# Optimization experiments

Measured on AMD Instinct MI355X. Metric: run time of the kernel, lower is better.

Reference implementation:

```python
import jax, jax.numpy as jnp
import numpy as np

N = 50000      # nodes
E = 800000     # edges (before self loops)
IN = 128       # input feature dim
HID = 64       # hidden channels per head
H = 4          # heads
OUT = 1        # final out channels
D1 = H * HID   # 256, concat feature dim
NEG_SLOPE = 0.2


def _p(k, shape):
    return jax.random.normal(k, shape, jnp.float32) * 0.1


def setup_inputs() -> dict:
    key = jax.random.key(0)
    ks = jax.random.split(key, 32)
    inp = {
        "x": jax.random.normal(ks[0], (N, IN), jnp.float32),
        "edge_index": jax.random.randint(ks[1], (2, E), 0, N, dtype=jnp.int32),
        "batch": jnp.zeros((N,), jnp.int32),
    }
    # layer 0: GATConv(IN -> HID, heads=H, concat) ; Linear(IN -> H*HID)
    inp["cW0"] = _p(ks[2], (IN, H * HID)); inp["cas0"] = _p(ks[3], (H, HID))
    inp["cad0"] = _p(ks[4], (H, HID));     inp["cb0"] = jnp.zeros((D1,), jnp.float32)
    inp["lW0"] = _p(ks[5], (IN, D1));      inp["lb0"] = jnp.zeros((D1,), jnp.float32)
    # layer 1: GATConv(D1 -> HID, heads=H, concat) ; Linear(D1 -> D1)
    inp["cW1"] = _p(ks[6], (D1, H * HID)); inp["cas1"] = _p(ks[7], (H, HID))
    inp["cad1"] = _p(ks[8], (H, HID));     inp["cb1"] = jnp.zeros((D1,), jnp.float32)
    inp["lW1"] = _p(ks[9], (D1, D1));      inp["lb1"] = jnp.zeros((D1,), jnp.float32)
    # layer 2: GATConv(D1 -> OUT, heads=H, concat=False -> mean) ; Linear(D1 -> OUT)
    inp["cW2"] = _p(ks[10], (D1, H * OUT)); inp["cas2"] = _p(ks[11], (H, OUT))
    inp["cad2"] = _p(ks[12], (H, OUT));     inp["cb2"] = jnp.zeros((OUT,), jnp.float32)
    inp["lW2"] = _p(ks[13], (D1, OUT));     inp["lb2"] = jnp.zeros((OUT,), jnp.float32)
    return inp


def gat_conv(x, W, att_src, att_dst, bias, src, dst, out_c, concat):
    """PyG-style GATConv with self loops already included in (src, dst)."""
    n = x.shape[0]
    xl = (x @ W).reshape(n, H, out_c)                  # [N,H,C]
    a_s = (xl * att_src).sum(-1)                       # [N,H]
    a_d = (xl * att_dst).sum(-1)                       # [N,H]
    e = jax.nn.leaky_relu(a_s[src] + a_d[dst], NEG_SLOPE)   # [Et,H]
    # numerically stable segment softmax over destination nodes
    e_max = jax.ops.segment_max(e, dst, num_segments=n)
    ex = jnp.exp(e - e_max[dst])
    denom = jax.ops.segment_sum(ex, dst, num_segments=n)
    alpha = ex / (denom[dst] + 1e-16)                  # [Et,H]
    msg = xl[src] * alpha[..., None]                   # [Et,H,C]
    out = jax.ops.segment_sum(msg, dst, num_segments=n)  # [N,H,C]
    out = out.reshape(n, H * out_c) if concat else out.mean(axis=1)
    return out + bias


def _forward(x, edge_index,
             cW0, cas0, cad0, cb0, lW0, lb0,
             cW1, cas1, cad1, cb1, lW1, lb1,
             cW2, cas2, cad2, cb2, lW2, lb2):
    n = x.shape[0]
    loop = jnp.arange(n, dtype=edge_index.dtype)
    src = jnp.concatenate([edge_index[0], loop])
    dst = jnp.concatenate([edge_index[1], loop])
    h = jax.nn.elu(gat_conv(x, cW0, cas0, cad0, cb0, src, dst, HID, True) + (x @ lW0 + lb0))
    h = jax.nn.elu(gat_conv(h, cW1, cas1, cad1, cb1, src, dst, HID, True) + (h @ lW1 + lb1))
    return gat_conv(h, cW2, cas2, cad2, cb2, src, dst, OUT, False) + (h @ lW2 + lb2)


def reference(x, edge_index, batch,
              cW0, cas0, cad0, cb0, lW0, lb0,
              cW1, cas1, cad1, cb1, lW1, lb1,
              cW2, cas2, cad2, cb2, lW2, lb2):
    return _forward(x, edge_index,
                    cW0, cas0, cad0, cb0, lW0, lb0,
                    cW1, cas1, cad1, cb1, lW1, lb1,
                    cW2, cas2, cad2, cb2, lW2, lb2)
```

## Files before the change

### kernel.cpp

```cpp
#include <hip/hip_runtime.h>
#include <cstddef>
#include <cstdint>

#define NN 50000
#define EE 800000
#define ET_ (EE + NN)

typedef __attribute__((ext_vector_type(8))) short bf16x8;
typedef __attribute__((ext_vector_type(4))) float f32x4;

__device__ __forceinline__ float lrelu_(float x) { return x > 0.f ? x : 0.2f * x; }
__device__ __forceinline__ float elu_(float x)   { return x > 0.f ? x : (__expf(x) - 1.f); }
__device__ __forceinline__ short f2bf(float f) {
    unsigned u = __float_as_uint(f);
    unsigned r = (u + 0x7fffu + ((u >> 16) & 1u)) >> 16;
    return (short)r;
}
__device__ __forceinline__ float bflo(unsigned u) { return __uint_as_float(u << 16); }
__device__ __forceinline__ float bfhi(unsigned u) { return __uint_as_float(u & 0xffff0000u); }
__device__ __forceinline__ float bfs(short s) { return __uint_as_float(((unsigned)(unsigned short)s) << 16); }

#define GL16(gp, lp) __builtin_amdgcn_global_load_lds( \
    (const __attribute__((address_space(1))) unsigned int*)(gp), \
    (__attribute__((address_space(3))) unsigned int*)(lp), 16, 0, 0)


__global__ __launch_bounds__(256) void prep_all(const float* __restrict__ x,
                                                const float* __restrict__ cW0, const float* __restrict__ lW0,
                                                const float* __restrict__ cW1, const float* __restrict__ lW1,
                                                const int* __restrict__ ei, int* __restrict__ deg,
                                                short* __restrict__ xb, short* __restrict__ Wt0,
                                                short* __restrict__ Wt1) {
    int i = blockIdx.x * 256 + threadIdx.x;
    if (i < 1600000) {
        float4 v = *(const float4*)(x + (size_t)i * 4);
        short4 o;
        o.x = f2bf(v.x); o.y = f2bf(v.y); o.z = f2bf(v.z); o.w = f2bf(v.w);
        *(short4*)(xb + (size_t)i * 4) = o;
        return;
    }
    i -= 1600000;
    if (i < 512 * 128) {
        int n = i >> 7, k = i & 127;
        float v = (n < 256) ? cW0[k * 256 + n] : lW0[k * 256 + (n - 256)];
        Wt0[i] = f2bf(v);
        return;
    }
    i -= 512 * 128;
    if (i < 512 * 256) {
        int n = i >> 8, k = i & 255;
        float v = (n < 256) ? cW1[k * 256 + n] : lW1[k * 256 + (n - 256)];
        Wt1[i] = f2bf(v);
        return;
    }
    i -= 512 * 256;
    if (i < ET_) {
        int d = (i < EE) ? ei[EE + i] : (i - EE);
        atomicAdd(&deg[d], 1);
    }
}


__global__ __launch_bounds__(1024) void alloc_scan(const int* __restrict__ deg, int* __restrict__ rowptr,
                                                   int* __restrict__ gcnt, int n) {
    __shared__ int s[1024];
    __shared__ int basesh;
    int tid = threadIdx.x;
    int gid = blockIdx.x * 1024 + tid;
    int v = (gid < n) ? deg[gid] : 0;
    s[tid] = v;
    __syncthreads();
    for (int off = 1; off < 1024; off <<= 1) {
        int t = (tid >= off) ? s[tid - off] : 0;
        __syncthreads();
        s[tid] += t;
        __syncthreads();
    }
    if (tid == 1023) basesh = atomicAdd(gcnt, s[1023]);
    __syncthreads();
    if (gid < n) rowptr[gid] = basesh + s[tid] - v;
}

__global__ __launch_bounds__(256) void scatter_k(const int* __restrict__ ei,
                                                 const int* __restrict__ rowptr,
                                                 int* __restrict__ cursor,
                                                 int* __restrict__ csr_src) {
    int e = blockIdx.x * blockDim.x + threadIdx.x;
    if (e >= ET_) return;
    int s, d;
    if (e < EE) { s = ei[e]; d = ei[EE + e]; } else { s = e - EE; d = e - EE; }
    int pos = atomicAdd(&cursor[d], 1);
    csr_src[rowptr[d] + pos] = s;
}


__global__ __launch_bounds__(256) void gemm_bf16(const short* __restrict__ A,
                                                 const short* __restrict__ Wt,
                                                 const float* __restrict__ biasLin,
                                                 const float* __restrict__ attS,
                                                 const float* __restrict__ attD,
                                                 short* __restrict__ XLb,
                                                 short* __restrict__ Hlinb,
                                                 float* __restrict__ AS,
                                                 float* __restrict__ AD,
                                                 int M, int K) {
    __shared__ short smem[4][128 * 32];
    const int tid = threadIdx.x;
    const int lane = tid & 63;
    const int wid = tid >> 6;
    const int bm = blockIdx.x * 128;
    const int col0 = blockIdx.y * 128;
    const int wr = wid >> 1, wc = wid & 1;

    f32x4 acc[4][4];
#pragma unroll
    for (int i = 0; i < 4; ++i)
#pragma unroll
        for (int j = 0; j < 4; ++j) acc[i][j] = (f32x4){0.f, 0.f, 0.f, 0.f};

    const int lrow = lane & 15, lk = lane >> 4;

    auto stage = [&](int b, int kk) {
#pragma unroll
        for (int it = 0; it < 2; ++it) {
            const int flat = tid + it * 256;
            const int row = flat >> 2, slot = flat & 3;
            const int ss = slot ^ (row & 3);
            int ar = bm + row; ar = (ar < M) ? ar : (M - 1);
            GL16(A + (size_t)ar * K + kk + ss * 8, &smem[b][flat * 8]);
            GL16(Wt + (size_t)(col0 + row) * K + kk + ss * 8, &smem[2 + b][flat * 8]);
        }
    };

    stage(0, 0);
    int cur = 0;
    for (int k0 = 0; k0 < K; k0 += 32) {
        __syncthreads();
        if (k0 + 32 < K) stage(cur ^ 1, k0 + 32);
        bf16x8 af[4], bfr[4];
#pragma unroll
        for (int mi = 0; mi < 4; ++mi) {
            const int r = wr * 64 + mi * 16 + lrow;
            af[mi] = *(const bf16x8*)(&smem[cur][(r * 4 + (lk ^ (r & 3))) * 8]);
        }
#pragma unroll
        for (int ni = 0; ni < 4; ++ni) {
            const int c = wc * 64 + ni * 16 + lrow;
            bfr[ni] = *(const bf16x8*)(&smem[2 + cur][(c * 4 + (lk ^ (c & 3))) * 8]);
        }
#pragma unroll
        for (int mi = 0; mi < 4; ++mi)
#pragma unroll
            for (int ni = 0; ni < 4; ++ni)
                acc[mi][ni] = __builtin_amdgcn_mfma_f32_16x16x32_bf16(af[mi], bfr[ni], acc[mi][ni], 0, 0, 0);
        cur ^= 1;
    }

    __syncthreads();
    short* Ct = &smem[0][0];
    const bool isLin = (col0 >= 256);
    float bni[4] = {0.f, 0.f, 0.f, 0.f};
    if (isLin) {
#pragma unroll
        for (int ni = 0; ni < 4; ++ni)
            bni[ni] = biasLin[col0 - 256 + wc * 64 + ni * 16 + lrow];
    }
    const int lrow4 = lk * 4;
#pragma unroll
    for (int mi = 0; mi < 4; ++mi) {
#pragma unroll
        for (int ni = 0; ni < 4; ++ni) {
            const int col_l = wc * 64 + ni * 16 + lrow;
#pragma unroll
            for (int rr = 0; rr < 4; ++rr) {
                const int row_l = wr * 64 + mi * 16 + lrow4 + rr;
                const int idx = (row_l * 128 + col_l) ^ (((row_l >> 2) & 3) << 4);
                Ct[idx] = f2bf(acc[mi][ni][rr] + bni[ni]);
            }
        }
    }
    __syncthreads();

    short* outp = isLin ? Hlinb : XLb;
    const int gcol0 = isLin ? (col0 - 256) : col0;
    const int seg = tid & 15;
    float4 sA0, sA1, sD0, sD1;
    if (!isLin) {
        sA0 = *(const float4*)(attS + col0 + seg * 8);
        sA1 = *(const float4*)(attS + col0 + seg * 8 + 4);
        sD0 = *(const float4*)(attD + col0 + seg * 8);
        sD1 = *(const float4*)(attD + col0 + seg * 8 + 4);
    }
#pragma unroll
    for (int rr8 = 0; rr8 < 8; ++rr8) {
        const int flat = tid + rr8 * 256;
        const int row = flat >> 4;
        const int sidx = (row * 128 + seg * 8) ^ (((row >> 2) & 3) << 4);
        const int grow = bm + row;
        bf16x8 vv = *(const bf16x8*)(Ct + sidx);
        if (grow < M)
            *(bf16x8*)(outp + (size_t)grow * 256 + gcol0 + seg * 8) = vv;
        if (!isLin) {
            float f0 = bfs(vv[0]), f1 = bfs(vv[1]), f2 = bfs(vv[2]), f3 = bfs(vv[3]);
            float f4 = bfs(vv[4]), f5 = bfs(vv[5]), f6 = bfs(vv[6]), f7 = bfs(vv[7]);
            float sp = f0 * sA0.x + f1 * sA0.y + f2 * sA0.z + f3 * sA0.w
                     + f4 * sA1.x + f5 * sA1.y + f6 * sA1.z + f7 * sA1.w;
            float dp = f0 * sD0.x + f1 * sD0.y + f2 * sD0.z + f3 * sD0.w
                     + f4 * sD1.x + f5 * sD1.y + f6 * sD1.z + f7 * sD1.w;
            sp += __shfl_xor(sp, 1); dp += __shfl_xor(dp, 1);
            sp += __shfl_xor(sp, 2); dp += __shfl_xor(dp, 2);
            sp += __shfl_xor(sp, 4); dp += __shfl_xor(dp, 4);
            if ((seg & 7) == 0 && grow < M) {
                const int hh = (col0 >> 6) + (seg >> 3);
                AS[grow * 4 + hh] = sp;
                AD[grow * 4 + hh] = dp;
            }
        }
    }
}


__global__ __launch_bounds__(256) void gat_agg(const short* __restrict__ XLb,
                                               const float* __restrict__ AS,
                                               const float* __restrict__ AD,
                                               const int* __restrict__ rowptr,
                                               const int* __restrict__ degarr,
                                               const int* __restrict__ csr_src,
                                               const float* __restrict__ cb,
                                               const short* __restrict__ Hlinb,
                                               short* __restrict__ Hb,
                                               const float* __restrict__ cW2,
                                               const float* __restrict__ lW2,
                                               const float* __restrict__ lb2,
                                               float* __restrict__ XL2,
                                               float* __restrict__ LIN2,
                                               int n_nodes) {
    __shared__ int   sIdx[4][64];
    __shared__ float sExT[4][4][72];

    const int tid = threadIdx.x;
    const int lane = tid & 63;
    const int w = tid >> 6;
    const int n = blockIdx.x * 4 + w;
    if (n >= n_nodes) return;

    const int rs = rowptr[n];
    const int deg = degarr[n];
    const float4 ad4 = *(const float4*)(AD + n * 4);

    const int half = lane >> 5;
    const int l32 = lane & 31;
    const int ch0 = l32 * 8;
    const int h = l32 >> 3;

    float4 acc0 = make_float4(0.f, 0.f, 0.f, 0.f);
    float4 acc1 = make_float4(0.f, 0.f, 0.f, 0.f);
    float d0 = 0.f, d1 = 0.f, d2 = 0.f, d3 = 0.f;

    auto ACC = [&](const uint4& q, float e) {
        acc0.x += e * bflo(q.x); acc0.y += e * bfhi(q.x);
        acc0.z += e * bflo(q.y); acc0.w += e * bfhi(q.y);
        acc1.x += e * bflo(q.z); acc1.y += e * bfhi(q.z);
        acc1.z += e * bflo(q.w); acc1.w += e * bfhi(q.w);
    };

    if (deg <= 64) {
        int sv = 0;
        float c0 = -1e30f, c1 = -1e30f, c2 = -1e30f, c3 = -1e30f;
        if (lane < deg) {
            sv = csr_src[rs + lane];
            float4 a = *(const float4*)(AS + sv * 4);
            c0 = lrelu_(a.x + ad4.x); c1 = lrelu_(a.y + ad4.y);
            c2 = lrelu_(a.z + ad4.z); c3 = lrelu_(a.w + ad4.w);
        }
        float m0 = c0, m1 = c1, m2 = c2, m3 = c3;
#pragma unroll
        for (int off = 32; off > 0; off >>= 1) {
            m0 = fmaxf(m0, __shfl_xor(m0, off));
            m1 = fmaxf(m1, __shfl_xor(m1, off));
            m2 = fmaxf(m2, __shfl_xor(m2, off));
            m3 = fmaxf(m3, __shfl_xor(m3, off));
        }
        float e0 = 0.f, e1 = 0.f, e2 = 0.f, e3 = 0.f;
        if (lane < deg) {
            e0 = __expf(c0 - m0); e1 = __expf(c1 - m1);
            e2 = __expf(c2 - m2); e3 = __expf(c3 - m3);
        }
        sIdx[w][lane] = sv;
        sExT[w][0][lane] = e0; sExT[w][1][lane] = e1;
        sExT[w][2][lane] = e2; sExT[w][3][lane] = e3;
        d0 = e0; d1 = e1; d2 = e2; d3 = e3;
        __builtin_amdgcn_wave_barrier();

        const int cpad = (deg + 1) & ~1;
        int j = 0;
        for (; j + 16 <= cpad; j += 16) {
            int jj[8]; int ss[8]; float ee[8]; uint4 qq[8];
#pragma unroll
            for (int u = 0; u < 8; ++u) { jj[u] = j + 2 * u + half; ss[u] = sIdx[w][jj[u]]; ee[u] = sExT[w][h][jj[u]]; }
#pragma unroll
            for (int u = 0; u < 8; ++u) qq[u] = *(const uint4*)(XLb + (size_t)ss[u] * 256 + ch0);
#pragma unroll
            for (int u = 0; u < 8; ++u) ACC(qq[u], ee[u]);
        }
        for (; j + 8 <= cpad; j += 8) {
            int ja = j + half, jb = j + 2 + half, jc = j + 4 + half, jd = j + 6 + half;
            int sa = sIdx[w][ja], sb = sIdx[w][jb], sc = sIdx[w][jc], sd = sIdx[w][jd];
            float ea = sExT[w][h][ja], eb = sExT[w][h][jb];
            float ec = sExT[w][h][jc], ed = sExT[w][h][jd];
            uint4 qa = *(const uint4*)(XLb + (size_t)sa * 256 + ch0);
            uint4 qb = *(const uint4*)(XLb + (size_t)sb * 256 + ch0);
            uint4 qc = *(const uint4*)(XLb + (size_t)sc * 256 + ch0);
            uint4 qd = *(const uint4*)(XLb + (size_t)sd * 256 + ch0);
            ACC(qa, ea); ACC(qb, eb); ACC(qc, ec); ACC(qd, ed);
        }
        for (; j < cpad; j += 2) {
            int jj = j + half;
            int s = sIdx[w][jj];
            float e = sExT[w][h][jj];
            uint4 q = *(const uint4*)(XLb + (size_t)s * 256 + ch0);
            ACC(q, e);
        }
    } else {
        float m0 = -1e30f, m1 = -1e30f, m2 = -1e30f, m3 = -1e30f;
        for (int base = 0; base < deg; base += 64) {
            int idx = base + lane;
            if (idx < deg) {
                int s = csr_src[rs + idx];
                float4 a = *(const float4*)(AS + s * 4);
                m0 = fmaxf(m0, lrelu_(a.x + ad4.x));
                m1 = fmaxf(m1, lrelu_(a.y + ad4.y));
                m2 = fmaxf(m2, lrelu_(a.z + ad4.z));
                m3 = fmaxf(m3, lrelu_(a.w + ad4.w));
            }
        }
#pragma unroll
        for (int off = 32; off > 0; off >>= 1) {
            m0 = fmaxf(m0, __shfl_xor(m0, off));
            m1 = fmaxf(m1, __shfl_xor(m1, off));
            m2 = fmaxf(m2, __shfl_xor(m2, off));
            m3 = fmaxf(m3, __shfl_xor(m3, off));
        }
        for (int base = 0; base < deg; base += 64) {
            int cnt = deg - base; if (cnt > 64) cnt = 64;
            int idx = base + lane;
            int sv = 0;
            float e0 = 0.f, e1 = 0.f, e2 = 0.f, e3 = 0.f;
            if (idx < deg) {
                sv = csr_src[rs + idx];
                float4 a = *(const float4*)(AS + sv * 4);
                e0 = __expf(lrelu_(a.x + ad4.x) - m0);
                e1 = __expf(lrelu_(a.y + ad4.y) - m1);
                e2 = __expf(lrelu_(a.z + ad4.z) - m2);
                e3 = __expf(lrelu_(a.w + ad4.w) - m3);
            }
            sIdx[w][lane] = sv;
            sExT[w][0][lane] = e0; sExT[w][1][lane] = e1;
            sExT[w][2][lane] = e2; sExT[w][3][lane] = e3;
            d0 += e0; d1 += e1; d2 += e2; d3 += e3;
            __builtin_amdgcn_wave_barrier();
            int cpad = (cnt + 1) & ~1;
            for (int j = 0; j < cpad; j += 2) {
                int jj = j + half;
                int s = sIdx[w][jj];
                float e = sExT[w][h][jj];
                uint4 q = *(const uint4*)(XLb + (size_t)s * 256 + ch0);
                ACC(q, e);
            }
            __builtin_amdgcn_wave_barrier();
        }
    }

    acc0.x += __shfl_xor(acc0.x, 32); acc0.y += __shfl_xor(acc0.y, 32);
    acc0.z += __shfl_xor(acc0.z, 32); acc0.w += __shfl_xor(acc0.w, 32);
    acc1.x += __shfl_xor(acc1.x, 32); acc1.y += __shfl_xor(acc1.y, 32);
    acc1.z += __shfl_xor(acc1.z, 32); acc1.w += __shfl_xor(acc1.w, 32);
#pragma unroll
    for (int off = 32; off > 0; off >>= 1) {
        d0 += __shfl_xor(d0, off); d1 += __shfl_xor(d1, off);
        d2 += __shfl_xor(d2, off); d3 += __shfl_xor(d3, off);
    }
    float den = (h == 0) ? d0 : (h == 1) ? d1 : (h == 2) ? d2 : d3;
    float inv = 1.f / (den + 1e-16f);

    float v0 = 0.f, v1 = 0.f, v2 = 0.f, v3 = 0.f, v4 = 0.f, v5 = 0.f, v6 = 0.f, v7 = 0.f;
    if (lane < 32) {
        size_t o = (size_t)n * 256 + ch0;
        uint4 hq = *(const uint4*)(Hlinb + o);
        float4 cba = *(const float4*)(cb + ch0);
        float4 cbb = *(const float4*)(cb + ch0 + 4);
        v0 = elu_(acc0.x * inv + cba.x + bflo(hq.x));
        v1 = elu_(acc0.y * inv + cba.y + bfhi(hq.x));
        v2 = elu_(acc0.z * inv + cba.z + bflo(hq.y));
        v3 = elu_(acc0.w * inv + cba.w + bfhi(hq.y));
        v4 = elu_(acc1.x * inv + cbb.x + bflo(hq.z));
        v5 = elu_(acc1.y * inv + cbb.y + bfhi(hq.z));
        v6 = elu_(acc1.z * inv + cbb.z + bflo(hq.w));
        v7 = elu_(acc1.w * inv + cbb.w + bfhi(hq.w));
    }

    if (XL2 != nullptr) {
        float p0 = 0.f, p1 = 0.f, p2 = 0.f, p3 = 0.f, pl = 0.f;
        if (lane < 32) {
            const float vv[8] = {v0, v1, v2, v3, v4, v5, v6, v7};
            float4 lwa = *(const float4*)(lW2 + ch0);
            float4 lwb = *(const float4*)(lW2 + ch0 + 4);
            const float lw[8] = {lwa.x, lwa.y, lwa.z, lwa.w, lwb.x, lwb.y, lwb.z, lwb.w};
#pragma unroll
            for (int j = 0; j < 8; ++j) {
                float4 wv = *(const float4*)(cW2 + (ch0 + j) * 4);
                p0 += vv[j] * wv.x; p1 += vv[j] * wv.y;
                p2 += vv[j] * wv.z; p3 += vv[j] * wv.w;
                pl += vv[j] * lw[j];
            }
        }
#pragma unroll
        for (int off = 16; off > 0; off >>= 1) {
            p0 += __shfl_xor(p0, off); p1 += __shfl_xor(p1, off);
            p2 += __shfl_xor(p2, off); p3 += __shfl_xor(p3, off);
            pl += __shfl_xor(pl, off);
        }
        if (lane == 0) {
            *(float4*)(XL2 + n * 4) = make_float4(p0, p1, p2, p3);
            LIN2[n] = pl + lb2[0];
        }
    } else if (lane < 32) {
        size_t o = (size_t)n * 256 + ch0;
        uint4 ov;
        ov.x = (unsigned)(unsigned short)f2bf(v0) | ((unsigned)(unsigned short)f2bf(v1) << 16);
        ov.y = (unsigned)(unsigned short)f2bf(v2) | ((unsigned)(unsigned short)f2bf(v3) << 16);
        ov.z = (unsigned)(unsigned short)f2bf(v4) | ((unsigned)(unsigned short)f2bf(v5) << 16);
        ov.w = (unsigned)(unsigned short)f2bf(v6) | ((unsigned)(unsigned short)f2bf(v7) << 16);
        *(uint4*)(Hb + o) = ov;
    }
}


__global__ __launch_bounds__(256) void l2_agg(const float* __restrict__ XL2,
                                              const float* __restrict__ LIN2,
                                              const float* __restrict__ cas2,
                                              const float* __restrict__ cad2,
                                              const float* __restrict__ cb2,
                                              const int* __restrict__ rowptr,
                                              const int* __restrict__ degarr,
                                              const int* __restrict__ csr_src,
                                              float* __restrict__ out, int n_nodes) {
    int n = (blockIdx.x * blockDim.x + threadIdx.x) >> 6;
    int lane = threadIdx.x & 63;
    if (n >= n_nodes) return;
    int rs = rowptr[n], re = rs + degarr[n];
    float4 xn = *(const float4*)(XL2 + n * 4);
    float cs0 = cas2[0], cs1 = cas2[1], cs2 = cas2[2], cs3 = cas2[3];
    float cd0 = cad2[0], cd1 = cad2[1], cd2 = cad2[2], cd3 = cad2[3];
    float ad0 = xn.x * cd0, ad1 = xn.y * cd1, ad2 = xn.z * cd2, ad3 = xn.w * cd3;

    float m0 = -1e30f, m1 = -1e30f, m2 = -1e30f, m3 = -1e30f;
    for (int i = rs + lane; i < re; i += 64) {
        int s = csr_src[i];
        float4 xs = *(const float4*)(XL2 + s * 4);
        m0 = fmaxf(m0, lrelu_(xs.x * cs0 + ad0));
        m1 = fmaxf(m1, lrelu_(xs.y * cs1 + ad1));
        m2 = fmaxf(m2, lrelu_(xs.z * cs2 + ad2));
        m3 = fmaxf(m3, lrelu_(xs.w * cs3 + ad3));
    }
#pragma unroll
    for (int off = 32; off > 0; off >>= 1) {
        m0 = fmaxf(m0, __shfl_xor(m0, off));
        m1 = fmaxf(m1, __shfl_xor(m1, off));
        m2 = fmaxf(m2, __shfl_xor(m2, off));
        m3 = fmaxf(m3, __shfl_xor(m3, off));
    }

    float d0 = 0.f, d1 = 0.f, d2 = 0.f, d3 = 0.f;
    float t0 = 0.f, t1 = 0.f, t2 = 0.f, t3 = 0.f;
    for (int i = rs + lane; i < re; i += 64) {
        int s = csr_src[i];
        float4 xs = *(const float4*)(XL2 + s * 4);
        float e0 = __expf(lrelu_(xs.x * cs0 + ad0) - m0);
        float e1 = __expf(lrelu_(xs.y * cs1 + ad1) - m1);
        float e2 = __expf(lrelu_(xs.z * cs2 + ad2) - m2);
        float e3 = __expf(lrelu_(xs.w * cs3 + ad3) - m3);
        d0 += e0; d1 += e1; d2 += e2; d3 += e3;
        t0 += e0 * xs.x; t1 += e1 * xs.y; t2 += e2 * xs.z; t3 += e3 * xs.w;
    }
#pragma unroll
    for (int off = 32; off > 0; off >>= 1) {
        d0 += __shfl_xor(d0, off); d1 += __shfl_xor(d1, off);
        d2 += __shfl_xor(d2, off); d3 += __shfl_xor(d3, off);
        t0 += __shfl_xor(t0, off); t1 += __shfl_xor(t1, off);
        t2 += __shfl_xor(t2, off); t3 += __shfl_xor(t3, off);
    }
    if (lane == 0) {
        float r = 0.25f * (t0 / (d0 + 1e-16f) + t1 / (d1 + 1e-16f) +
                           t2 / (d2 + 1e-16f) + t3 / (d3 + 1e-16f));
        out[n] = r + cb2[0] + LIN2[n];
    }
}


extern "C" void kernel_launch(void* const* d_in, const int* in_sizes, int n_in,
                              void* d_out, int out_size, void* d_ws, size_t ws_size,
                              hipStream_t stream) {
    const float* x    = (const float*)d_in[0];
    const int*   ei   = (const int*)d_in[1];
    const float* cW0  = (const float*)d_in[3];
    const float* cas0 = (const float*)d_in[4];
    const float* cad0 = (const float*)d_in[5];
    const float* cb0  = (const float*)d_in[6];
    const float* lW0  = (const float*)d_in[7];
    const float* lb0  = (const float*)d_in[8];
    const float* cW1  = (const float*)d_in[9];
    const float* cas1 = (const float*)d_in[10];
    const float* cad1 = (const float*)d_in[11];
    const float* cb1  = (const float*)d_in[12];
    const float* lW1  = (const float*)d_in[13];
    const float* lb1  = (const float*)d_in[14];
    const float* cW2  = (const float*)d_in[15];
    const float* cas2 = (const float*)d_in[16];
    const float* cad2 = (const float*)d_in[17];
    const float* cb2  = (const float*)d_in[18];
    const float* lW2  = (const float*)d_in[19];
    const float* lb2  = (const float*)d_in[20];
    float* out = (float*)d_out;

    short* xb    = (short*)d_ws;
    short* XLb   = xb + 6400000;
    short* HAb   = XLb + 12800000;
    short* Hlinb = HAb + 12800000;
    short* Wt0   = Hlinb + 12800000;
    short* Wt1   = Wt0 + 65536;
    float* AS    = (float*)(Wt1 + 131072);
    float* AD    = AS + 200000;
    float* XL2   = AD + 200000;
    float* LIN2  = XL2 + 200000;
    int* deg     = (int*)(LIN2 + NN);
    int* cursor  = deg + NN;
    int* gcnt    = cursor + NN;
    int* rowptr  = gcnt + 4;
    int* csr_src = rowptr + NN;

    dim3 b256(256);
    dim3 gEdges((ET_ + 255) / 256);
    dim3 gNodesWave((NN + 3) / 4);

    hipMemsetAsync(deg, 0, (2 * (size_t)NN + 4) * sizeof(int), stream);
    prep_all<<<dim3(10339), b256, 0, stream>>>(x, cW0, lW0, cW1, lW1, ei, deg, xb, Wt0, Wt1);
    alloc_scan<<<dim3((NN + 1023) / 1024), dim3(1024), 0, stream>>>(deg, rowptr, gcnt, NN);
    scatter_k<<<gEdges, b256, 0, stream>>>(ei, rowptr, cursor, csr_src);

    dim3 gemmGrid((NN + 127) / 128, 4);

    gemm_bf16<<<gemmGrid, b256, 0, stream>>>(xb, Wt0, lb0, cas0, cad0, XLb, Hlinb, AS, AD, NN, 128);
    gat_agg<<<gNodesWave, b256, 0, stream>>>(XLb, AS, AD, rowptr, deg, csr_src, cb0, Hlinb,
                                             HAb, nullptr, nullptr, nullptr, nullptr, nullptr, NN);

    gemm_bf16<<<gemmGrid, b256, 0, stream>>>(HAb, Wt1, lb1, cas1, cad1, XLb, Hlinb, AS, AD, NN, 256);
    gat_agg<<<gNodesWave, b256, 0, stream>>>(XLb, AS, AD, rowptr, deg, csr_src, cb1, Hlinb,
                                             nullptr, cW2, lW2, lb2, XL2, LIN2, NN);

    l2_agg<<<gNodesWave, b256, 0, stream>>>(XL2, LIN2, cas2, cad2, cb2, rowptr, deg, csr_src, out, NN);
}
```

Baseline: 466.7 us.

## Split gat_agg into per-layer kernels, simplify gather loop, single-pass l2_agg

Splits the shared aggregation kernel into two specialized kernels (layer-0 bf16 output and layer-1 fused projection) built on a common inline core, which removes the runtime nullptr branch. It replaces the 16/8-wide unrolled gather loops with a single 2-edge-per-iteration loop to cut register pressure, and adds launch_bounds(256,8) to push occupancy. l2_agg gets a single-pass path for degree at most 64 that loads each neighbour once instead of twice. The trade is less memory-level parallelism per wave in the gather loop, with latency hidden by more resident waves instead.

Result: faster. 450.3 us (-3.5%).

```diff
diff --git a/kernel.cpp b/kernel.cpp
--- a/kernel.cpp
+++ b/kernel.cpp
@@ -220,49 +220,16 @@
 }
 
 
-__global__ __launch_bounds__(256) void gat_agg(const short* __restrict__ XLb,
-                                               const float* __restrict__ AS,
-                                               const float* __restrict__ AD,
-                                               const int* __restrict__ rowptr,
-                                               const int* __restrict__ degarr,
-                                               const int* __restrict__ csr_src,
-                                               const float* __restrict__ cb,
-                                               const short* __restrict__ Hlinb,
-                                               short* __restrict__ Hb,
-                                               const float* __restrict__ cW2,
-                                               const float* __restrict__ lW2,
-                                               const float* __restrict__ lb2,
-                                               float* __restrict__ XL2,
-                                               float* __restrict__ LIN2,
-                                               int n_nodes) {
-    __shared__ int   sIdx[4][64];
-    __shared__ float sExT[4][4][72];
-
-    const int tid = threadIdx.x;
-    const int lane = tid & 63;
-    const int w = tid >> 6;
-    const int n = blockIdx.x * 4 + w;
-    if (n >= n_nodes) return;
-
-    const int rs = rowptr[n];
-    const int deg = degarr[n];
-    const float4 ad4 = *(const float4*)(AD + n * 4);
-
-    const int half = lane >> 5;
-    const int l32 = lane & 31;
-    const int ch0 = l32 * 8;
-    const int h = l32 >> 3;
-
-    float4 acc0 = make_float4(0.f, 0.f, 0.f, 0.f);
-    float4 acc1 = make_float4(0.f, 0.f, 0.f, 0.f);
+__device__ __forceinline__ void agg_core(const short* __restrict__ XLb,
+                                         const float* __restrict__ AS,
+                                         const float4 ad4,
+                                         int rs, int deg,
+                                         const int* __restrict__ csr_src,
+                                         int w, int lane,
+                                         int (*sIdx)[64], float (*sExT)[4][72],
+                                         float4& acc0, float4& acc1, float& denOut,
+                                         int half, int l32, int ch0, int h) {
     float d0 = 0.f, d1 = 0.f, d2 = 0.f, d3 = 0.f;
-
-    auto ACC = [&](const uint4& q, float e) {
-        acc0.x += e * bflo(q.x); acc0.y += e * bfhi(q.x);
-        acc0.z += e * bflo(q.y); acc0.w += e * bfhi(q.y);
-        acc1.x += e * bflo(q.z); acc1.y += e * bfhi(q.z);
-        acc1.z += e * bflo(q.w); acc1.w += e * bfhi(q.w);
-    };
 
     if (deg <= 64) {
         int sv = 0;
@@ -293,33 +260,15 @@
         __builtin_amdgcn_wave_barrier();
 
         const int cpad = (deg + 1) & ~1;
-        int j = 0;
-        for (; j + 16 <= cpad; j += 16) {
-            int jj[8]; int ss[8]; float ee[8]; uint4 qq[8];
-#pragma unroll
-            for (int u = 0; u < 8; ++u) { jj[u] = j + 2 * u + half; ss[u] = sIdx[w][jj[u]]; ee[u] = sExT[w][h][jj[u]]; }
-#pragma unroll
-            for (int u = 0; u < 8; ++u) qq[u] = *(const uint4*)(XLb + (size_t)ss[u] * 256 + ch0);
-#pragma unroll
-            for (int u = 0; u < 8; ++u) ACC(qq[u], ee[u]);
-        }
-        for (; j + 8 <= cpad; j += 8) {
-            int ja = j + half, jb = j + 2 + half, jc = j + 4 + half, jd = j + 6 + half;
-            int sa = sIdx[w][ja], sb = sIdx[w][jb], sc = sIdx[w][jc], sd = sIdx[w][jd];
-            float ea = sExT[w][h][ja], eb = sExT[w][h][jb];
-            float ec = sExT[w][h][jc], ed = sExT[w][h][jd];
-            uint4 qa = *(const uint4*)(XLb + (size_t)sa * 256 + ch0);
-            uint4 qb = *(const uint4*)(XLb + (size_t)sb * 256 + ch0);
-            uint4 qc = *(const uint4*)(XLb + (size_t)sc * 256 + ch0);
-            uint4 qd = *(const uint4*)(XLb + (size_t)sd * 256 + ch0);
-            ACC(qa, ea); ACC(qb, eb); ACC(qc, ec); ACC(qd, ed);
-        }
-        for (; j < cpad; j += 2) {
+        for (int j = 0; j < cpad; j += 2) {
             int jj = j + half;
             int s = sIdx[w][jj];
             float e = sExT[w][h][jj];
-            uint4 q = *(const uint4*)(XLb + (size_t)s * 256 + ch0);
-            ACC(q, e);
+            const uint4 q = *(const uint4*)(XLb + (size_t)s * 256 + ch0);
+            acc0.x += e * bflo(q.x); acc0.y += e * bfhi(q.x);
+            acc0.z += e * bflo(q.y); acc0.w += e * bfhi(q.y);
+            acc1.x += e * bflo(q.z); acc1.y += e * bfhi(q.z);
+            acc1.z += e * bflo(q.w); acc1.w += e * bfhi(q.w);
         }
     } else {
         float m0 = -1e30f, m1 = -1e30f, m2 = -1e30f, m3 = -1e30f;
@@ -364,8 +313,11 @@
                 int jj = j + half;
                 int s = sIdx[w][jj];
                 float e = sExT[w][h][jj];
-                uint4 q = *(const uint4*)(XLb + (size_t)s * 256 + ch0);
-                ACC(q, e);
+                const uint4 q = *(const uint4*)(XLb + (size_t)s * 256 + ch0);
+                acc0.x += e * bflo(q.x); acc0.y += e * bfhi(q.x);
+                acc0.z += e * bflo(q.y); acc0.w += e * bfhi(q.y);
+                acc1.x += e * bflo(q.z); acc1.y += e * bfhi(q.z);
+                acc1.z += e * bflo(q.w); acc1.w += e * bfhi(q.w);
             }
             __builtin_amdgcn_wave_barrier();
         }
@@ -380,52 +332,52 @@
         d0 += __shfl_xor(d0, off); d1 += __shfl_xor(d1, off);
         d2 += __shfl_xor(d2, off); d3 += __shfl_xor(d3, off);
     }
-    float den = (h == 0) ? d0 : (h == 1) ? d1 : (h == 2) ? d2 : d3;
+    denOut = (h == 0) ? d0 : (h == 1) ? d1 : (h == 2) ? d2 : d3;
+}
+
+
+__global__ __launch_bounds__(256, 8) void gat_agg0(const short* __restrict__ XLb,
+                                                   const float* __restrict__ AS,
+                                                   const float* __restrict__ AD,
+                                                   const int* __restrict__ rowptr,
+                                                   const int* __restrict__ degarr,
+                                                   const int* __restrict__ csr_src,
+                                                   const float* __restrict__ cb,
+                                                   const short* __restrict__ Hlinb,
+                                                   short* __restrict__ Hb, int n_nodes) {
+    __shared__ int   sIdx[4][64];
+    __shared__ float sExT[4][4][72];
+    const int tid = threadIdx.x;
+    const int lane = tid & 63;
+    const int w = tid >> 6;
+    const int n = blockIdx.x * 4 + w;
+    if (n >= n_nodes) return;
+
+    const int rs = rowptr[n];
+    const int deg = degarr[n];
+    const float4 ad4 = *(const float4*)(AD + n * 4);
+    const int half = lane >> 5, l32 = lane & 31, ch0 = l32 * 8, h = l32 >> 3;
+
+    float4 acc0 = make_float4(0.f, 0.f, 0.f, 0.f);
+    float4 acc1 = make_float4(0.f, 0.f, 0.f, 0.f);
+    float den;
+    agg_core(XLb, AS, ad4, rs, deg, csr_src, w, lane, sIdx, sExT, acc0, acc1, den,
+             half, l32, ch0, h);
     float inv = 1.f / (den + 1e-16f);
 
-    float v0 = 0.f, v1 = 0.f, v2 = 0.f, v3 = 0.f, v4 = 0.f, v5 = 0.f, v6 = 0.f, v7 = 0.f;
     if (lane < 32) {
         size_t o = (size_t)n * 256 + ch0;
         uint4 hq = *(const uint4*)(Hlinb + o);
         float4 cba = *(const float4*)(cb + ch0);
         float4 cbb = *(const float4*)(cb + ch0 + 4);
-        v0 = elu_(acc0.x * inv + cba.x + bflo(hq.x));
-        v1 = elu_(acc0.y * inv + cba.y + bfhi(hq.x));
-        v2 = elu_(acc0.z * inv + cba.z + bflo(hq.y));
-        v3 = elu_(acc0.w * inv + cba.w + bfhi(hq.y));
-        v4 = elu_(acc1.x * inv + cbb.x + bflo(hq.z));
-        v5 = elu_(acc1.y * inv + cbb.y + bfhi(hq.z));
-        v6 = elu_(acc1.z * inv + cbb.z + bflo(hq.w));
-        v7 = elu_(acc1.w * inv + cbb.w + bfhi(hq.w));
-    }
-
-    if (XL2 != nullptr) {
-        float p0 = 0.f, p1 = 0.f, p2 = 0.f, p3 = 0.f, pl = 0.f;
-        if (lane < 32) {
-            const float vv[8] = {v0, v1, v2, v3, v4, v5, v6, v7};
-            float4 lwa = *(const float4*)(lW2 + ch0);
-            float4 lwb = *(const float4*)(lW2 + ch0 + 4);
-            const float lw[8] = {lwa.x, lwa.y, lwa.z, lwa.w, lwb.x, lwb.y, lwb.z, lwb.w};
-#pragma unroll
-            for (int j = 0; j < 8; ++j) {
-                float4 wv = *(const float4*)(cW2 + (ch0 + j) * 4);
-                p0 += vv[j] * wv.x; p1 += vv[j] * wv.y;
-                p2 += vv[j] * wv.z; p3 += vv[j] * wv.w;
-                pl += vv[j] * lw[j];
-            }
-        }
-#pragma unroll
-        for (int off = 16; off > 0; off >>= 1) {
-            p0 += __shfl_xor(p0, off); p1 += __shfl_xor(p1, off);
-            p2 += __shfl_xor(p2, off); p3 += __shfl_xor(p3, off);
-            pl += __shfl_xor(pl, off);
-        }
-        if (lane == 0) {
-            *(float4*)(XL2 + n * 4) = make_float4(p0, p1, p2, p3);
-            LIN2[n] = pl + lb2[0];
-        }
-    } else if (lane < 32) {
-        size_t o = (size_t)n * 256 + ch0;
+        float v0 = elu_(acc0.x * inv + cba.x + bflo(hq.x));
+        float v1 = elu_(acc0.y * inv + cba.y + bfhi(hq.x));
+        float v2 = elu_(acc0.z * inv + cba.z + bflo(hq.y));
+        float v3 = elu_(acc0.w * inv + cba.w + bfhi(hq.y));
+        float v4 = elu_(acc1.x * inv + cbb.x + bflo(hq.z));
+        float v5 = elu_(acc1.y * inv + cbb.y + bfhi(hq.z));
+        float v6 = elu_(acc1.z * inv + cbb.z + bflo(hq.w));
+        float v7 = elu_(acc1.w * inv + cbb.w + bfhi(hq.w));
         uint4 ov;
         ov.x = (unsigned)(unsigned short)f2bf(v0) | ((unsigned)(unsigned short)f2bf(v1) << 16);
         ov.y = (unsigned)(unsigned short)f2bf(v2) | ((unsigned)(unsigned short)f2bf(v3) << 16);
@@ -436,52 +388,151 @@
 }
 
 
-__global__ __launch_bounds__(256) void l2_agg(const float* __restrict__ XL2,
-                                              const float* __restrict__ LIN2,
-                                              const float* __restrict__ cas2,
-                                              const float* __restrict__ cad2,
-                                              const float* __restrict__ cb2,
-                                              const int* __restrict__ rowptr,
-                                              const int* __restrict__ degarr,
-                                              const int* __restrict__ csr_src,
-                                              float* __restrict__ out, int n_nodes) {
+__global__ __launch_bounds__(256, 8) void gat_agg1(const short* __restrict__ XLb,
+                                                   const float* __restrict__ AS,
+                                                   const float* __restrict__ AD,
+                                                   const int* __restrict__ rowptr,
+                                                   const int* __restrict__ degarr,
+                                                   const int* __restrict__ csr_src,
+                                                   const float* __restrict__ cb,
+                                                   const short* __restrict__ Hlinb,
+                                                   const float* __restrict__ cW2,
+                                                   const float* __restrict__ lW2,
+                                                   const float* __restrict__ lb2,
+                                                   float* __restrict__ XL2,
+                                                   float* __restrict__ LIN2, int n_nodes) {
+    __shared__ int   sIdx[4][64];
+    __shared__ float sExT[4][4][72];
+    const int tid = threadIdx.x;
+    const int lane = tid & 63;
+    const int w = tid >> 6;
+    const int n = blockIdx.x * 4 + w;
+    if (n >= n_nodes) return;
+
+    const int rs = rowptr[n];
+    const int deg = degarr[n];
+    const float4 ad4 = *(const float4*)(AD + n * 4);
+    const int half = lane >> 5, l32 = lane & 31, ch0 = l32 * 8, h = l32 >> 3;
+
+    float4 acc0 = make_float4(0.f, 0.f, 0.f, 0.f);
+    float4 acc1 = make_float4(0.f, 0.f, 0.f, 0.f);
+    float den;
+    agg_core(XLb, AS, ad4, rs, deg, csr_src, w, lane, sIdx, sExT, acc0, acc1, den,
+             half, l32, ch0, h);
+    float inv = 1.f / (den + 1e-16f);
+
+    float p0 = 0.f, p1 = 0.f, p2 = 0.f, p3 = 0.f, pl = 0.f;
+    if (lane < 32) {
+        size_t o = (size_t)n * 256 + ch0;
+        uint4 hq = *(const uint4*)(Hlinb + o);
+        float4 cba = *(const float4*)(cb + ch0);
+        float4 cbb = *(const float4*)(cb + ch0 + 4);
+        float vv[8];
+        vv[0] = elu_(acc0.x * inv + cba.x + bflo(hq.x));
+        vv[1] = elu_(acc0.y * inv + cba.y + bfhi(hq.x));
+        vv[2] = elu_(acc0.z * inv + cba.z + bflo(hq.y));
+        vv[3] = elu_(acc0.w * inv + cba.w + bfhi(hq.y));
+        vv[4] = elu_(acc1.x * inv + cbb.x + bflo(hq.z));
+        vv[5] = elu_(acc1.y * inv + cbb.y + bfhi(hq.z));
+        vv[6] = elu_(acc1.z * inv + cbb.z + bflo(hq.w));
+        vv[7] = elu_(acc1.w * inv + cbb.w + bfhi(hq.w));
+        float4 lwa = *(const float4*)(lW2 + ch0);
+        float4 lwb = *(const float4*)(lW2 + ch0 + 4);
+        const float lw[8] = {lwa.x, lwa.y, lwa.z, lwa.w, lwb.x, lwb.y, lwb.z, lwb.w};
+#pragma unroll
+        for (int j = 0; j < 8; ++j) {
+            float4 wv = *(const float4*)(cW2 + (ch0 + j) * 4);
+            p0 += vv[j] * wv.x; p1 += vv[j] * wv.y;
+            p2 += vv[j] * wv.z; p3 += vv[j] * wv.w;
+            pl += vv[j] * lw[j];
+        }
+    }
+#pragma unroll
+    for (int off = 16; off > 0; off >>= 1) {
+        p0 += __shfl_xor(p0, off); p1 += __shfl_xor(p1, off);
+        p2 += __shfl_xor(p2, off); p3 += __shfl_xor(p3, off);
+        pl += __shfl_xor(pl, off);
+    }
+    if (lane == 0) {
+        *(float4*)(XL2 + n * 4) = make_float4(p0, p1, p2, p3);
+        LIN2[n] = pl + lb2[0];
+    }
+}
+
+
+__global__ __launch_bounds__(256, 8) void l2_agg(const float* __restrict__ XL2,
+                                                 const float* __restrict__ LIN2,
+                                                 const float* __restrict__ cas2,
+                                                 const float* __restrict__ cad2,
+                                                 const float* __restrict__ cb2,
+                                                 const int* __restrict__ rowptr,
+                                                 const int* __restrict__ degarr,
+                                                 const int* __restrict__ csr_src,
+                                                 float* __restrict__ out, int n_nodes) {
     int n = (blockIdx.x * blockDim.x + threadIdx.x) >> 6;
     int lane = threadIdx.x & 63;
     if (n >= n_nodes) return;
-    int rs = rowptr[n], re = rs + degarr[n];
+    int rs = rowptr[n];
+    int deg = degarr[n];
     float4 xn = *(const float4*)(XL2 + n * 4);
     float cs0 = cas2[0], cs1 = cas2[1], cs2 = cas2[2], cs3 = cas2[3];
     float cd0 = cad2[0], cd1 = cad2[1], cd2 = cad2[2], cd3 = cad2[3];
     float ad0 = xn.x * cd0, ad1 = xn.y * cd1, ad2 = xn.z * cd2, ad3 = xn.w * cd3;
 
-    float m0 = -1e30f, m1 = -1e30f, m2 = -1e30f, m3 = -1e30f;
-    for (int i = rs + lane; i < re; i += 64) {
-        int s = csr_src[i];
-        float4 xs = *(const float4*)(XL2 + s * 4);
-        m0 = fmaxf(m0, lrelu_(xs.x * cs0 + ad0));
-        m1 = fmaxf(m1, lrelu_(xs.y * cs1 + ad1));
-        m2 = fmaxf(m2, lrelu_(xs.z * cs2 + ad2));
-        m3 = fmaxf(m3, lrelu_(xs.w * cs3 + ad3));
-    }
-#pragma unroll
-    for (int off = 32; off > 0; off >>= 1) {
-        m0 = fmaxf(m0, __shfl_xor(m0, off));
-        m1 = fmaxf(m1, __shfl_xor(m1, off));
-        m2 = fmaxf(m2, __shfl_xor(m2, off));
-        m3 = fmaxf(m3, __shfl_xor(m3, off));
-    }
-
     float d0 = 0.f, d1 = 0.f, d2 = 0.f, d3 = 0.f;
     float t0 = 0.f, t1 = 0.f, t2 = 0.f, t3 = 0.f;
-    for (int i = rs + lane; i < re; i += 64) {
-        int s = csr_src[i];
-        float4 xs = *(const float4*)(XL2 + s * 4);
-        float e0 = __expf(lrelu_(xs.x * cs0 + ad0) - m0);
-        float e1 = __expf(lrelu_(xs.y * cs1 + ad1) - m1);
-        float e2 = __expf(lrelu_(xs.z * cs2 + ad2) - m2);
-        float e3 = __expf(lrelu_(xs.w * cs3 + ad3) - m3);
-        d0 += e0; d1 += e1; d2 += e2; d3 += e3;
-        t0 += e0 * xs.x; t1 += e1 * xs.y; t2 += e2 * xs.z; t3 += e3 * xs.w;
+
+    if (deg <= 64) {
+        float4 xs = make_float4(0.f, 0.f, 0.f, 0.f);
+        float c0 = -1e30f, c1 = -1e30f, c2 = -1e30f, c3 = -1e30f;
+        if (lane < deg) {
+            int s = csr_src[rs + lane];
+            xs = *(const float4*)(XL2 + s * 4);
+            c0 = lrelu_(xs.x * cs0 + ad0); c1 = lrelu_(xs.y * cs1 + ad1);
+            c2 = lrelu_(xs.z * cs2 + ad2); c3 = lrelu_(xs.w * cs3 + ad3);
+        }
+        float m0 = c0, m1 = c1, m2 = c2, m3 = c3;
+#pragma unroll
+        for (int off = 32; off > 0; off >>= 1) {
+            m0 = fmaxf(m0, __shfl_xor(m0, off));
+            m1 = fmaxf(m1, __shfl_xor(m1, off));
+            m2 = fmaxf(m2, __shfl_xor(m2, off));
+            m3 = fmaxf(m3, __shfl_xor(m3, off));
+        }
+        if (lane < deg) {
+            float e0 = __expf(c0 - m0), e1 = __expf(c1 - m1);
+            float e2 = __expf(c2 - m2), e3 = __expf(c3 - m3);
+            d0 = e0; d1 = e1; d2 = e2; d3 = e3;
+            t0 = e0 * xs.x; t1 = e1 * xs.y; t2 = e2 * xs.z; t3 = e3 * xs.w;
+        }
+    } else {
+        int re = rs + deg;
+        float m0 = -1e30f, m1 = -1e30f, m2 = -1e30f, m3 = -1e30f;
+        for (int i = rs + lane; i < re; i += 64) {
+            int s = csr_src[i];
+            float4 xs = *(const float4*)(XL2 + s * 4);
+            m0 = fmaxf(m0, lrelu_(xs.x * cs0 + ad0));
+            m1 = fmaxf(m1, lrelu_(xs.y * cs1 + ad1));
+            m2 = fmaxf(m2, lrelu_(xs.z * cs2 + ad2));
+            m3 = fmaxf(m3, lrelu_(xs.w * cs3 + ad3));
+        }
+#pragma unroll
+        for (int off = 32; off > 0; off >>= 1) {
+            m0 = fmaxf(m0, __shfl_xor(m0, off));
+            m1 = fmaxf(m1, __shfl_xor(m1, off));
+            m2 = fmaxf(m2, __shfl_xor(m2, off));
+            m3 = fmaxf(m3, __shfl_xor(m3, off));
+        }
+        for (int i = rs + lane; i < re; i += 64) {
+            int s = csr_src[i];
+            float4 xs = *(const float4*)(XL2 + s * 4);
+            float e0 = __expf(lrelu_(xs.x * cs0 + ad0) - m0);
+            float e1 = __expf(lrelu_(xs.y * cs1 + ad1) - m1);
+            float e2 = __expf(lrelu_(xs.z * cs2 + ad2) - m2);
+            float e3 = __expf(lrelu_(xs.w * cs3 + ad3) - m3);
+            d0 += e0; d1 += e1; d2 += e2; d3 += e3;
+            t0 += e0 * xs.x; t1 += e1 * xs.y; t2 += e2 * xs.z; t3 += e3 * xs.w;
+        }
     }
 #pragma unroll
     for (int off = 32; off > 0; off >>= 1) {
@@ -551,12 +602,11 @@
     dim3 gemmGrid((NN + 127) / 128, 4);
 
     gemm_bf16<<<gemmGrid, b256, 0, stream>>>(xb, Wt0, lb0, cas0, cad0, XLb, Hlinb, AS, AD, NN, 128);
-    gat_agg<<<gNodesWave, b256, 0, stream>>>(XLb, AS, AD, rowptr, deg, csr_src, cb0, Hlinb,
-                                             HAb, nullptr, nullptr, nullptr, nullptr, nullptr, NN);
+    gat_agg0<<<gNodesWave, b256, 0, stream>>>(XLb, AS, AD, rowptr, deg, csr_src, cb0, Hlinb, HAb, NN);
 
     gemm_bf16<<<gemmGrid, b256, 0, stream>>>(HAb, Wt1, lb1, cas1, cad1, XLb, Hlinb, AS, AD, NN, 256);
-    gat_agg<<<gNodesWave, b256, 0, stream>>>(XLb, AS, AD, rowptr, deg, csr_src, cb1, Hlinb,
-                                             nullptr, cW2, lW2, lb2, XL2, LIN2, NN);
+    gat_agg1<<<gNodesWave, b256, 0, stream>>>(XLb, AS, AD, rowptr, deg, csr_src, cb1, Hlinb,
+                                              cW2, lW2, lb2, XL2, LIN2, NN);
 
     l2_agg<<<gNodesWave, b256, 0, stream>>>(XL2, LIN2, cas2, cad2, cb2, rowptr, deg, csr_src, out, NN);
 }
```
